# Kernel optimization log

Hardware: AMD Instinct MI355X
Metric: run time of the kernel (lower is better)

Reference implementation:

```python
import jax, jax.numpy as jnp
import numpy as np

B_, L_, H_, P_ = 8, 4096, 512, 256
DT_MIN, DT_MAX = 1e-3, 1e-1


def setup_inputs() -> dict:
    key = jax.random.key(0)
    ks = jax.random.split(key, 6)
    input_sequence = jax.random.normal(ks[0], (B_, L_, H_), jnp.float32)
    # Stable diagonal SSM eigenvalues (HiPPO-like): negative real, spread imaginary
    Lambda_re = -0.5 * jnp.ones((P_,), jnp.float32)
    Lambda_im = jnp.pi * jnp.arange(P_, dtype=jnp.float32)
    # B, C stored as real arrays with trailing real/imag channel, as in the module
    B = jax.random.normal(ks[1], (P_, H_, 2), jnp.float32) / np.sqrt(2.0 * H_)
    C = jax.random.normal(ks[2], (H_, P_, 2), jnp.float32) / np.sqrt(float(P_))
    D = jax.random.normal(ks[3], (H_,), jnp.float32)
    log_step = jax.random.uniform(ks[4], (P_,), jnp.float32,
                                  float(np.log(DT_MIN)), float(np.log(DT_MAX)))
    return dict(input_sequence=input_sequence, Lambda_re=Lambda_re,
                Lambda_im=Lambda_im, B=B, C=C, D=D, log_step=log_step)


def _scan_ssm(Lambda_bar, Bu):
    """Diagonal linear recurrence x_k = Lambda_bar * x_{k-1} + Bu_k via parallel scan.
    Lambda_bar: (P,) complex64; Bu: (L, P) complex64 -> xs: (L, P) complex64."""
    A = jnp.broadcast_to(Lambda_bar, Bu.shape)

    def binop(e_i, e_j):
        a_i, b_i = e_i
        a_j, b_j = e_j
        return a_j * a_i, a_j * b_i + b_j

    _, xs = jax.lax.associative_scan(binop, (A, Bu))
    return xs


def reference(input_sequence, Lambda_re, Lambda_im, B, C, D, log_step):
    # complex parameters (conj_sym=True, clip_eigs=False, zoh discretization)
    Lambda = (Lambda_re + 1j * Lambda_im).astype(jnp.complex64)        # (P,)
    B_tilde = (B[..., 0] + 1j * B[..., 1]).astype(jnp.complex64)       # (P, H)
    C_tilde = (C[..., 0] + 1j * C[..., 1]).astype(jnp.complex64)       # (H, P)
    step = jnp.exp(log_step)                                           # (P,)
    # ZOH: Lambda_bar = exp(Lambda*dt); B_bar = Lambda^{-1}(Lambda_bar - I) B
    Lambda_bar = jnp.exp(Lambda * step)                                # (P,)
    B_bar = ((1.0 / Lambda) * (Lambda_bar - 1.0))[:, None] * B_tilde   # (P, H)
    # project inputs into state space: (B, L, P)
    Bu = jnp.einsum('blh,ph->blp', input_sequence.astype(jnp.complex64), B_bar)
    xs = jax.vmap(lambda bu: _scan_ssm(Lambda_bar, bu))(Bu)            # (B, L, P)
    state = xs[:, -1, :]                                               # (B, P)
    # conj_sym=True -> output uses 2 * Re(C x)
    ys = 2.0 * jnp.einsum('blp,hp->blh', xs, C_tilde).real             # (B, L, H)
    out = ys + D * input_sequence                                      # D-skip
    return out, state
```

## Files before the change

### kernel.cpp

```cpp
#include <hip/hip_runtime.h>
#include <hip/hip_bf16.h>

#define Hh 512
#define Pp 256
#define Ll 4096
#define Bb 8
#define BL (Bb*Ll)
#define Sc 64
#define NC 64

typedef __attribute__((ext_vector_type(8))) __bf16 bf16x8;
typedef __attribute__((ext_vector_type(4))) float  floatx4;

#define LAM_OFF     0
#define LAMS64D_OFF 512
#define B1G_OFF     1024
#define B3G_OFF     (B1G_OFF + 65536)
#define UB16_OFF    (B3G_OFF + 65536)
#define BUB_OFF     (UB16_OFF + 4194304)
#define XSB_OFF     (BUB_OFF + 4194304)
#define AGG_OFF     (XSB_OFF + 4194304)

#define LAMS16D_OFF XSB_OFF
#define AGG16_OFF   (XSB_OFF + 512)

#define OUT_ELEMS 16777216

#define GLL16(g, l) __builtin_amdgcn_global_load_lds( \
    (const __attribute__((address_space(1))) void*)(g), \
    (__attribute__((address_space(3))) void*)(l), 16, 0, 0)

#define BAR_LGKM()  asm volatile("s_waitcnt lgkmcnt(0)\n\ts_barrier" ::: "memory")
#define BAR_VMN(n)  asm volatile("s_waitcnt vmcnt(" #n ")\n\ts_barrier" ::: "memory")

__device__ __forceinline__ float2 cmul(float2 a, float2 b) {
    return make_float2(a.x*b.x - a.y*b.y, a.x*b.y + a.y*b.x);
}
__device__ __forceinline__ void cfma(float2& acc, float2 a, float2 b) {
    acc.x = fmaf(a.x, b.x, acc.x); acc.x = fmaf(-a.y, b.y, acc.x);
    acc.y = fmaf(a.x, b.y, acc.y); acc.y = fmaf( a.y, b.x, acc.y);
}

__global__ void prep(const float* __restrict__ u,
                     const float* __restrict__ Bmat, const float* __restrict__ Cmat,
                     const float* __restrict__ Lre, const float* __restrict__ Lim,
                     const float* __restrict__ logstep, float2* __restrict__ ws) {
    int bid = blockIdx.x;
    if (bid < 8192) {
        long i = ((long)bid * 256 + threadIdx.x) * 8;
        float4 v0 = *(const float4*)(u + i);
        float4 v1 = *(const float4*)(u + i + 4);
        __align__(16) __hip_bfloat162 t[4];
        t[0] = __float22bfloat162_rn(make_float2(v0.x, v0.y));
        t[1] = __float22bfloat162_rn(make_float2(v0.z, v0.w));
        t[2] = __float22bfloat162_rn(make_float2(v1.x, v1.y));
        t[3] = __float22bfloat162_rn(make_float2(v1.z, v1.w));
        *(bf16x8*)((__hip_bfloat16*)(ws + UB16_OFF) + i) = *(const bf16x8*)t;
    } else if (bid < 8704) {
        int idx = (bid - 8192) * 256 + threadIdx.x;
        int p = idx >> 9, h = idx & 511;
        double lr = (double)Lre[p], li = (double)Lim[p];
        double st = exp((double)logstep[p]);
        double a  = lr * st, th = li * st;
        double er = exp(a);
        double lamr = er * cos(th), lami = er * sin(th);
        double nr = lamr - 1.0, ni = lami;
        double den = lr*lr + li*li;
        float gx = (float)((nr*lr + ni*li)/den), gy = (float)((ni*lr - nr*li)/den);
        float2 b = ((const float2*)Bmat)[idx];
        float re = gx*b.x - gy*b.y;
        float im = gx*b.y + gy*b.x;
        __hip_bfloat16* B1 = (__hip_bfloat16*)(ws + B1G_OFF);
        B1[(2*p)*512 + h]   = __float2bfloat16(re);
        B1[(2*p+1)*512 + h] = __float2bfloat16(im);
    } else if (bid < 9216) {
        int idx = (bid - 8704) * 256 + threadIdx.x;
        int h = idx >> 8, p = idx & 255;
        float2 c = ((const float2*)Cmat)[idx];
        __hip_bfloat162* B3 = (__hip_bfloat162*)(ws + B3G_OFF);
        B3[h*256 + p] = __float22bfloat162_rn(make_float2(2.f*c.x, -2.f*c.y));
    } else {
        int p = threadIdx.x;
        double lr = (double)Lre[p], li = (double)Lim[p];
        double st = exp((double)logstep[p]);
        double a  = lr * st, th = li * st;
        double er = exp(a);
        ws[LAM_OFF + p] = make_float2((float)(er*cos(th)), (float)(er*sin(th)));
        double er64 = exp(64.0 * a), th64 = 64.0 * th;
        ((double2*)(ws + LAMS64D_OFF))[p] = make_double2(er64*cos(th64), er64*sin(th64));
        double er16 = exp(16.0 * a), th16 = 16.0 * th;
        ((double2*)(ws + LAMS16D_OFF))[p] = make_double2(er16*cos(th16), er16*sin(th16));
    }
}

#define STAGE(buf, kt) do { \
    _Pragma("unroll") \
    for (int h_ = 0; h_ < 2; ++h_) { \
        _Pragma("unroll") \
        for (int r_ = 0; r_ < 2; ++r_) { \
            GLL16(aSrc + (h_*128 + r_*64)*1024 + (kt)*128, \
                  ldsSt + (buf)*65536 + h_*16384 + r_*8192); \
            GLL16(bSrc + (h_*128 + r_*64)*1024 + (kt)*128, \
                  ldsSt + (buf)*65536 + 32768 + h_*16384 + r_*8192); \
        } \
    } \
} while (0)

__global__ __launch_bounds__(512, 2)
void gemm1(const __hip_bfloat16* __restrict__ A,
           const __hip_bfloat16* __restrict__ B,
           void* __restrict__ Cout,
           const float2* __restrict__ lamTab,
           float2* __restrict__ aggOut,
           float2* __restrict__ agg16Out) {
    __shared__ __align__(16) char lds[131072];
    const int tid = threadIdx.x;
    const int w = tid >> 6, l = tid & 63;

    const int idx = blockIdx.x;
    const int swz = (idx & 7) * 32 + (idx >> 3);
    const int mt = swz >> 1, nt = swz & 1;
    const long M0 = (long)mt * 256;
    const int  N0 = nt * 256;

    const int rA  = l >> 3;
    const int csw = ((l & 7) ^ rA) * 16;
    const char* aSrc = (const char*)A + (M0 + w*8 + rA) * 1024 + csw;
    const char* bSrc = (const char*)B + (long)(N0 + w*8 + rA) * 1024 + csw;
    char* ldsSt = lds + w*1024 + l*16;

    const int quad = l >> 4, ml = l & 15, m7 = ml & 7;
    const int wm = w & 1, wn = w >> 1;
    const int o0 = ((quad    ) ^ m7) * 16;
    const int o1 = ((quad + 4) ^ m7) * 16;
    const char* aRd = lds + wm*16384 + ml*128;
    const char* bRd = lds + 32768 + wn*8192 + ml*128;

    floatx4 acc[8][4];
    #pragma unroll
    for (int i = 0; i < 8; ++i)
        #pragma unroll
        for (int j = 0; j < 4; ++j) acc[i][j] = (floatx4)0.f;

    STAGE(0, 0);
    STAGE(1, 1);
    BAR_VMN(8);

    #pragma unroll
    for (int t = 0; t < 8; ++t) {
        const int tb = (t & 1) * 65536;
        {
            bf16x8 af[8], bfr[4];
            #pragma unroll
            for (int fm = 0; fm < 8; ++fm)
                af[fm] = *(const bf16x8*)(aRd + tb + fm*2048 + o0);
            #pragma unroll
            for (int fn = 0; fn < 4; ++fn)
                bfr[fn] = *(const bf16x8*)(bRd + tb + fn*2048 + o0);
            __builtin_amdgcn_s_setprio(1);
            #pragma unroll
            for (int fm = 0; fm < 8; ++fm)
                #pragma unroll
                for (int fn = 0; fn < 4; ++fn)
                    acc[fm][fn] = __builtin_amdgcn_mfma_f32_16x16x32_bf16(
                        af[fm], bfr[fn], acc[fm][fn], 0, 0, 0);
            __builtin_amdgcn_s_setprio(0);
        }
        {
            bf16x8 af[8], bfr[4];
            #pragma unroll
            for (int fm = 0; fm < 8; ++fm)
                af[fm] = *(const bf16x8*)(aRd + tb + fm*2048 + o1);
            #pragma unroll
            for (int fn = 0; fn < 4; ++fn)
                bfr[fn] = *(const bf16x8*)(bRd + tb + fn*2048 + o1);
            BAR_LGKM();
            if (t + 2 < 8) STAGE(t & 1, t + 2);
            __builtin_amdgcn_sched_barrier(0);
            __builtin_amdgcn_s_setprio(1);
            #pragma unroll
            for (int fm = 0; fm < 8; ++fm)
                #pragma unroll
                for (int fn = 0; fn < 4; ++fn)
                    acc[fm][fn] = __builtin_amdgcn_mfma_f32_16x16x32_bf16(
                        af[fm], bfr[fn], acc[fm][fn], 0, 0, 0);
            __builtin_amdgcn_s_setprio(0);
        }
        if (t < 6)       BAR_VMN(8);
        else if (t == 6) BAR_VMN(0);
    }

    __syncthreads();
    __hip_bfloat16* ldsC = (__hip_bfloat16*)lds;
    const int b   = (int)(M0 >> 12);
    const int gc0 = (int)((M0 >> 6) & 63);
    #pragma unroll
    for (int fn = 0; fn < 4; ++fn) {
        const int col = N0 + wn*64 + fn*16 + ml;
        const int cl  = wn*64 + fn*16 + ml;
        const int p = col >> 1;
        const float2 lam = lamTab[p];
        const float2 one = make_float2(1.f, 0.f);
        const float2 l2  = cmul(lam, lam);
        const float2 l3  = cmul(l2, lam);
        const float2 l4  = cmul(l2, l2);
        const float2 l8  = cmul(l4, l4);
        const float2 l12 = cmul(l8, l4);
        const float2 l16 = cmul(l8, l8);
        const float2 l32 = cmul(l16, l16);
        const float2 l48 = cmul(l32, l16);
        const float2 P4q = (quad==3) ? one : (quad==2) ? l4 : (quad==1) ? l8 : l12;
        #pragma unroll
        for (int c = 0; c < 2; ++c) {
            float2 sc = make_float2(0.f, 0.f);
            #pragma unroll
            for (int a = 0; a < 4; ++a) {
                const int fm = c*4 + a;
                float vr[4];
                #pragma unroll
                for (int reg = 0; reg < 4; ++reg) {
                    const int rl = wm*128 + fm*16 + quad*4 + reg;
                    __hip_bfloat16 hv = __float2bfloat16(acc[fm][fn][reg]);
                    ldsC[rl*256 + cl] = hv;
                    vr[reg] = __bfloat162float(hv);
                }
                float2 s;
                s.x = fmaf(l3.x, vr[0], fmaf(l2.x, vr[1], fmaf(lam.x, vr[2], vr[3])));
                s.y = fmaf(l3.y, vr[0], fmaf(l2.y, vr[1], lam.y * vr[2]));
                const float2 p16 = (a==3) ? one : (a==2) ? l16 : (a==1) ? l32 : l48;
                cfma(sc, cmul(p16, P4q), s);
                float2 tq = cmul(P4q, s);
                tq.x += __shfl_xor(tq.x, 16); tq.y += __shfl_xor(tq.y, 16);
                tq.x += __shfl_xor(tq.x, 32); tq.y += __shfl_xor(tq.y, 32);
                const float tox = __shfl_xor(tq.x, 1);
                const float toy = __shfl_xor(tq.y, 1);
                if (quad == 0 && (ml & 1) == 0)
                    agg16Out[((size_t)((b*NC + gc0 + wm*2 + c)*4 + a))*Pp + p] =
                        make_float2(tq.x - toy, tq.y + tox);
            }
            sc.x += __shfl_xor(sc.x, 16); sc.y += __shfl_xor(sc.y, 16);
            sc.x += __shfl_xor(sc.x, 32); sc.y += __shfl_xor(sc.y, 32);
            const float ox = __shfl_xor(sc.x, 1);
            const float oy = __shfl_xor(sc.y, 1);
            if (quad == 0 && (ml & 1) == 0) {
                aggOut[(b*NC + gc0 + wm*2 + c) * Pp + p] =
                    make_float2(sc.x - oy, sc.y + ox);
            }
        }
    }
    __syncthreads();
    {
        const int rr = tid >> 5;
        const int cb = (tid & 31) * 16;
        #pragma unroll
        for (int pass = 0; pass < 16; ++pass) {
            const int r = pass * 16 + rr;
            *(float4*)((char*)Cout + (M0 + r) * 1024 + (long)N0 * 2 + cb) =
                *(const float4*)(lds + r * 512 + cb);
        }
    }
}

#define STAGEA2(buf, kt) do { \
    _Pragma("unroll") \
    for (int h_ = 0; h_ < 2; ++h_) { \
        _Pragma("unroll") \
        for (int r_ = 0; r_ < 2; ++r_) { \
            GLL16(aSrc + (h_*128 + r_*64)*1024 + (kt)*128, \
                  ldsA + (buf)*32768 + h_*16384 + r_*8192); \
        } \
    } \
} while (0)
#define STAGEB2(buf, kt) do { \
    _Pragma("unroll") \
    for (int h_ = 0; h_ < 2; ++h_) { \
        _Pragma("unroll") \
        for (int r_ = 0; r_ < 2; ++r_) { \
            GLL16(bSrc + (h_*128 + r_*64)*1024 + (kt)*128, \
                  ldsB + (buf)*32768 + h_*16384 + r_*8192); \
        } \
    } \
} while (0)

#define SCAN_TILE(ktC, bufA) do { \
    const int s16_ = tid >> 5; \
    const float2 lam_ = lamK[ktC]; \
    float2 x_ = carry16L[s16_*256 + (ktC)*32 + p5g]; \
    char* base_ = lds + (bufA)*32768; \
    float2 v_[16]; \
    _Pragma("unroll") \
    for (int jj_ = 0; jj_ < 16; ++jj_) { \
        const int j_ = (s16_ << 4) + jj_; \
        v_[jj_] = __bfloat1622float2(*(const __hip_bfloat162*)(base_ + j_*128 + \
            ((((p5g >> 2) ^ (j_ & 7)) << 4) | ((p5g & 3) << 2)))); \
    } \
    _Pragma("unroll") \
    for (int jj_ = 0; jj_ < 16; ++jj_) { \
        const int j_ = (s16_ << 4) + jj_; \
        float nr_ = fmaf(lam_.x, x_.x, v_[jj_].x); nr_ = fmaf(-lam_.y, x_.y, nr_); \
        float ni_ = fmaf(lam_.x, x_.y, v_[jj_].y); ni_ = fmaf( lam_.y, x_.x, ni_); \
        x_.x = nr_; x_.y = ni_; \
        *(__hip_bfloat162*)(base_ + j_*128 + \
            ((((p5g >> 2) ^ (j_ & 7)) << 4) | ((p5g & 3) << 2))) = \
            __float22bfloat162_rn(x_); \
    } \
    if (s16_ == 15 && gc0 == 60 && nt == 0) { \
        out[OUT_ELEMS + b * Pp + (ktC)*32 + p5g] = x_.x; \
        out[OUT_ELEMS + Bb * Pp + b * Pp + (ktC)*32 + p5g] = x_.y; \
    } \
} while (0)

__global__ __launch_bounds__(512, 2)
void gemm2f(const __hip_bfloat16* __restrict__ A,
            const __hip_bfloat16* __restrict__ Bg,
            float* __restrict__ out,
            const __hip_bfloat16* __restrict__ ub,
            const float* __restrict__ Dv,
            const float2* __restrict__ lamTab,
            const double2* __restrict__ lam64,
            const double2* __restrict__ lam16,
            const float2* __restrict__ agg,
            const float2* __restrict__ agg16) {
    __shared__ __align__(16) char lds[163840];
    const int tid = threadIdx.x;
    const int w = tid >> 6, l = tid & 63;
    const int idx = blockIdx.x;
    const int swz = (idx & 7) * 32 + (idx >> 3);
    const int mt = swz >> 1, nt = swz & 1;
    const long M0 = (long)mt * 256;
    const int  N0 = nt * 256;
    const int b   = (int)(M0 >> 12);
    const int gc0 = (int)((M0 >> 6) & 63);

    const int rA  = l >> 3;
    const int csw = ((l & 7) ^ rA) * 16;
    const char* aSrc = (const char*)A + (M0 + w*8 + rA) * 1024 + csw;
    const char* bSrc = (const char*)Bg + (long)(N0 + w*8 + rA) * 1024 + csw;
    char* ldsA = lds + w*1024 + l*16;
    char* ldsB = lds + 65536 + w*1024 + l*16;

    const int quad = l >> 4, ml = l & 15, m7 = ml & 7;
    const int wm = w & 1, wn = w >> 1;
    const int o0 = ((quad    ) ^ m7) * 16;
    const int o1 = ((quad + 4) ^ m7) * 16;
    const char* aRd = lds + wm*16384 + ml*128;
    const char* bRd = lds + 65536 + wn*8192 + ml*128;
    float2* carry16L = (float2*)(lds + 131072);

    const int p5g = tid & 31;
    float2 lamK[8];
    #pragma unroll
    for (int kt = 0; kt < 8; ++kt) lamK[kt] = lamTab[kt*32 + p5g];

    STAGEA2(0, 0); STAGEB2(0, 0);
    STAGEA2(1, 1); STAGEB2(1, 1);

    if (tid < 256) {
        const int p = tid;
        const double2 l64 = lam64[p];
        const double2 l16 = lam16[p];
        double cr = 0.0, ci = 0.0;
        for (int cp = 0; cp + 4 <= gc0; cp += 4) {
            float2 a0 = agg[(b*NC + cp    ) * Pp + p];
            float2 a1 = agg[(b*NC + cp + 1) * Pp + p];
            float2 a2 = agg[(b*NC + cp + 2) * Pp + p];
            float2 a3 = agg[(b*NC + cp + 3) * Pp + p];
            double nr, ni;
            nr = fma(l64.x, cr, (double)a0.x); nr = fma(-l64.y, ci, nr);
            ni = fma(l64.x, ci, (double)a0.y); ni = fma( l64.y, cr, ni); cr = nr; ci = ni;
            nr = fma(l64.x, cr, (double)a1.x); nr = fma(-l64.y, ci, nr);
            ni = fma(l64.x, ci, (double)a1.y); ni = fma( l64.y, cr, ni); cr = nr; ci = ni;
            nr = fma(l64.x, cr, (double)a2.x); nr = fma(-l64.y, ci, nr);
            ni = fma(l64.x, ci, (double)a2.y); ni = fma( l64.y, cr, ni); cr = nr; ci = ni;
            nr = fma(l64.x, cr, (double)a3.x); nr = fma(-l64.y, ci, nr);
            ni = fma(l64.x, ci, (double)a3.y); ni = fma( l64.y, cr, ni); cr = nr; ci = ni;
        }
        #pragma unroll
        for (int ch = 0; ch < 4; ++ch) {
            carry16L[(ch*4 + 0)*256 + p] = make_float2((float)cr, (float)ci);
            double scr = cr, sci = ci;
            #pragma unroll
            for (int sq = 1; sq < 4; ++sq) {
                float2 a16 = agg16[((size_t)((b*NC + gc0 + ch)*4 + (sq-1)))*Pp + p];
                double nr = fma(l16.x, scr, (double)a16.x); nr = fma(-l16.y, sci, nr);
                double ni = fma(l16.x, sci, (double)a16.y); ni = fma( l16.y, scr, ni);
                scr = nr; sci = ni;
                carry16L[(ch*4 + sq)*256 + p] = make_float2((float)scr, (float)sci);
            }
            if (ch < 3) {
                float2 a = agg[(b*NC + gc0 + ch) * Pp + p];
                double nr = fma(l64.x, cr, (double)a.x); nr = fma(-l64.y, ci, nr);
                double ni = fma(l64.x, ci, (double)a.y); ni = fma( l64.y, cr, ni);
                cr = nr; ci = ni;
            }
        }
    }
    asm volatile("s_waitcnt vmcnt(8) lgkmcnt(0)\n\ts_barrier" ::: "memory");
    SCAN_TILE(0, 0);
    BAR_LGKM();

    floatx4 acc[8][4];
    #pragma unroll
    for (int i = 0; i < 8; ++i)
        #pragma unroll
        for (int j = 0; j < 4; ++j) acc[i][j] = (floatx4)0.f;

    #pragma unroll
    for (int kt = 0; kt < 8; ++kt) {
        const int cb = kt & 1;
        const int tb = cb * 32768;
        {
            bf16x8 af[8], bfr[4];
            #pragma unroll
            for (int fm = 0; fm < 8; ++fm)
                af[fm] = *(const bf16x8*)(aRd + tb + fm*2048 + o0);
            #pragma unroll
            for (int fn = 0; fn < 4; ++fn)
                bfr[fn] = *(const bf16x8*)(bRd + tb + fn*2048 + o0);
            __builtin_amdgcn_s_setprio(1);
            #pragma unroll
            for (int fm = 0; fm < 8; ++fm)
                #pragma unroll
                for (int fn = 0; fn < 4; ++fn)
                    acc[fm][fn] = __builtin_amdgcn_mfma_f32_16x16x32_bf16(
                        af[fm], bfr[fn], acc[fm][fn], 0, 0, 0);
            __builtin_amdgcn_s_setprio(0);
        }
        {
            bf16x8 af[8], bfr[4];
            #pragma unroll
            for (int fm = 0; fm < 8; ++fm)
                af[fm] = *(const bf16x8*)(aRd + tb + fm*2048 + o1);
            #pragma unroll
            for (int fn = 0; fn < 4; ++fn)
                bfr[fn] = *(const bf16x8*)(bRd + tb + fn*2048 + o1);
            BAR_LGKM();
            if (kt + 2 < 8) { STAGEA2(cb, kt + 2); STAGEB2(cb, kt + 2); }
            __builtin_amdgcn_sched_barrier(0);
            __builtin_amdgcn_s_setprio(1);
            #pragma unroll
            for (int fm = 0; fm < 8; ++fm)
                #pragma unroll
                for (int fn = 0; fn < 4; ++fn)
                    acc[fm][fn] = __builtin_amdgcn_mfma_f32_16x16x32_bf16(
                        af[fm], bfr[fn], acc[fm][fn], 0, 0, 0);
            __builtin_amdgcn_s_setprio(0);
        }
        if (kt < 6)       { BAR_VMN(8); SCAN_TILE(kt + 1, cb ^ 1); BAR_LGKM(); }
        else if (kt == 6) { BAR_VMN(0); SCAN_TILE(7, cb ^ 1); BAR_LGKM(); }
    }

    #pragma unroll
    for (int fm = 0; fm < 8; ++fm)
        #pragma unroll
        for (int fn = 0; fn < 4; ++fn) {
            const int col = N0 + wn*64 + fn*16 + ml;
            const float d = Dv[col];
            #pragma unroll
            for (int reg = 0; reg < 4; ++reg) {
                const long row = M0 + wm*128 + fm*16 + quad*4 + reg;
                const long o = row * 512 + col;
                out[o] = acc[fm][fn][reg] + d * __bfloat162float(ub[o]);
            }
        }
}

extern "C" void kernel_launch(void* const* d_in, const int* in_sizes, int n_in,
                              void* d_out, int out_size, void* d_ws, size_t ws_size,
                              hipStream_t stream) {
    const float* u       = (const float*)d_in[0];
    const float* Lre     = (const float*)d_in[1];
    const float* Lim     = (const float*)d_in[2];
    const float* Bmat    = (const float*)d_in[3];
    const float* Cmat    = (const float*)d_in[4];
    const float* Dv      = (const float*)d_in[5];
    const float* logstep = (const float*)d_in[6];
    float*  out = (float*)d_out;
    float2* ws  = (float2*)d_ws;

    prep<<<9217, 256, 0, stream>>>(u, Bmat, Cmat, Lre, Lim, logstep, ws);

    gemm1<<<256, 512, 0, stream>>>(
        (const __hip_bfloat16*)(ws + UB16_OFF),
        (const __hip_bfloat16*)(ws + B1G_OFF),
        (void*)(ws + BUB_OFF),
        (const float2*)(ws + LAM_OFF),
        (float2*)(ws + AGG_OFF),
        (float2*)(ws + AGG16_OFF));

    gemm2f<<<256, 512, 0, stream>>>(
        (const __hip_bfloat16*)(ws + BUB_OFF),
        (const __hip_bfloat16*)(ws + B3G_OFF),
        out,
        (const __hip_bfloat16*)(ws + UB16_OFF), Dv,
        (const float2*)(ws + LAM_OFF),
        (const double2*)(ws + LAMS64D_OFF),
        (const double2*)(ws + LAMS16D_OFF),
        (const float2*)(ws + AGG_OFF),
        (const float2*)(ws + AGG16_OFF));
}
```

Baseline: 185.4 us.

## Overlap scan tile with MFMA and stage epilogue through LDS for coalesced stores

The scan of the next tile is moved inside the second MFMA sub-step, so it is issued before the matrix multiplies rather than after them. This should let scan work overlap with MFMA execution. The output epilogue now writes accumulators to LDS one half-block at a time, then reads them back row-wise so the D-skip fused store uses float4 writes and 8-byte bf16 loads instead of scattered scalar accesses. This adds extra barriers and LDS traffic, and it reuses the LDS buffer, which could be a hazard if other data is still live there.

```diff
diff --git a/kernel.cpp b/kernel.cpp
--- a/kernel.cpp
+++ b/kernel.cpp
@@ -437,6 +437,8 @@
             BAR_LGKM();
             if (kt + 2 < 8) { STAGEA2(cb, kt + 2); STAGEB2(cb, kt + 2); }
             __builtin_amdgcn_sched_barrier(0);
+            if (kt < 6)       { BAR_VMN(8); SCAN_TILE(kt + 1, cb ^ 1); }
+            else if (kt == 6) { BAR_VMN(0); SCAN_TILE(7, cb ^ 1); }
             __builtin_amdgcn_s_setprio(1);
             #pragma unroll
             for (int fm = 0; fm < 8; ++fm)
@@ -445,24 +447,46 @@
                     acc[fm][fn] = __builtin_amdgcn_mfma_f32_16x16x32_bf16(
                         af[fm], bfr[fn], acc[fm][fn], 0, 0, 0);
             __builtin_amdgcn_s_setprio(0);
-        }
-        if (kt < 6)       { BAR_VMN(8); SCAN_TILE(kt + 1, cb ^ 1); BAR_LGKM(); }
-        else if (kt == 6) { BAR_VMN(0); SCAN_TILE(7, cb ^ 1); BAR_LGKM(); }
-    }
-
-    #pragma unroll
-    for (int fm = 0; fm < 8; ++fm)
+            if (kt < 7) BAR_LGKM();
+        }
+    }
+
+    __syncthreads();
+    float* ldsC = (float*)lds;
+    const int er = tid >> 6;
+    const int ec = (tid & 63) * 4;
+    #pragma unroll
+    for (int half = 0; half < 2; ++half) {
+        if (wm == half) {
+            #pragma unroll
+            for (int fm = 0; fm < 8; ++fm)
+                #pragma unroll
+                for (int fn = 0; fn < 4; ++fn) {
+                    const int cl = wn*64 + fn*16 + ml;
+                    #pragma unroll
+                    for (int reg = 0; reg < 4; ++reg)
+                        ldsC[(fm*16 + quad*4 + reg)*256 + cl] = acc[fm][fn][reg];
+                }
+        }
+        __syncthreads();
         #pragma unroll
-        for (int fn = 0; fn < 4; ++fn) {
-            const int col = N0 + wn*64 + fn*16 + ml;
-            const float d = Dv[col];
-            #pragma unroll
-            for (int reg = 0; reg < 4; ++reg) {
-                const long row = M0 + wm*128 + fm*16 + quad*4 + reg;
-                const long o = row * 512 + col;
-                out[o] = acc[fm][fn][reg] + d * __bfloat162float(ub[o]);
-            }
-        }
+        for (int g = 0; g < 16; ++g) {
+            const int rl = g*8 + er;
+            const long row = M0 + half*128 + rl;
+            float4 v = *(const float4*)(ldsC + rl*256 + ec);
+            const __hip_bfloat16* up = ub + row*512 + N0 + ec;
+            float2 f01 = __bfloat1622float2(*(const __hip_bfloat162*)up);
+            float2 f23 = __bfloat1622float2(*(const __hip_bfloat162*)(up + 2));
+            float4 dv = *(const float4*)(Dv + N0 + ec);
+            float4 o;
+            o.x = fmaf(dv.x, f01.x, v.x);
+            o.y = fmaf(dv.y, f01.y, v.y);
+            o.z = fmaf(dv.z, f23.x, v.z);
+            o.w = fmaf(dv.w, f23.y, v.w);
+            *(float4*)(out + row*512 + N0 + ec) = o;
+        }
+        __syncthreads();
+    }
 }
 
 extern "C" void kernel_launch(void* const* d_in, const int* in_sizes, int n_in,
```

After: 191.0 us. +3.0%, slower.

## Shrink gemm2f tiles to 128x128 and launch four times as many blocks

Applied to the files above, without the earlier changes.

The fused scan+GEMM kernel now uses 128x128 output tiles instead of 256x256, with 1024 blocks, half the LDS and launch bounds raised to 4 blocks per CU. The carry setup, staging, scan (now done by half the threads) and final-state write are all adjusted to the smaller 128-row chunk. This aims to fill the GPU better (256 blocks previously underfilled the CUs) and improve latency hiding. In exchange there is less operand reuse per block, more redundant carry-prefix computation across blocks, and only half the threads do the serial scan.

```diff
diff --git a/kernel.cpp b/kernel.cpp
--- a/kernel.cpp
+++ b/kernel.cpp
@@ -261,56 +261,50 @@
     }
 }
 
-#define STAGEA2(buf, kt) do { \
+#define STAGEA3(buf, kt) do { \
     _Pragma("unroll") \
     for (int h_ = 0; h_ < 2; ++h_) { \
+        GLL16(aSrc + (h_*64)*1024 + (kt)*128, ldsA + (buf)*16384 + h_*8192); \
+    } \
+} while (0)
+#define STAGEB3(buf, kt) do { \
+    _Pragma("unroll") \
+    for (int h_ = 0; h_ < 2; ++h_) { \
+        GLL16(bSrc + (h_*64)*1024 + (kt)*128, ldsB + (buf)*16384 + h_*8192); \
+    } \
+} while (0)
+
+#define SCAN3(ktC, bufA) do { \
+    if (tid < 256) { \
+        const int s16_ = tid >> 5;            \
+        const float2 lam_ = lamK[ktC]; \
+        float2 x_ = carry16L[s16_*256 + (ktC)*32 + p5g]; \
+        char* base_ = lds + (bufA)*16384; \
+        float2 v_[16]; \
         _Pragma("unroll") \
-        for (int r_ = 0; r_ < 2; ++r_) { \
-            GLL16(aSrc + (h_*128 + r_*64)*1024 + (kt)*128, \
-                  ldsA + (buf)*32768 + h_*16384 + r_*8192); \
+        for (int jj_ = 0; jj_ < 16; ++jj_) { \
+            const int j_ = (s16_ << 4) + jj_; \
+            v_[jj_] = __bfloat1622float2(*(const __hip_bfloat162*)(base_ + j_*128 + \
+                ((((p5g >> 2) ^ (j_ & 7)) << 4) | ((p5g & 3) << 2)))); \
+        } \
+        _Pragma("unroll") \
+        for (int jj_ = 0; jj_ < 16; ++jj_) { \
+            const int j_ = (s16_ << 4) + jj_; \
+            float nr_ = fmaf(lam_.x, x_.x, v_[jj_].x); nr_ = fmaf(-lam_.y, x_.y, nr_); \
+            float ni_ = fmaf(lam_.x, x_.y, v_[jj_].y); ni_ = fmaf( lam_.y, x_.x, ni_); \
+            x_.x = nr_; x_.y = ni_; \
+            *(__hip_bfloat162*)(base_ + j_*128 + \
+                ((((p5g >> 2) ^ (j_ & 7)) << 4) | ((p5g & 3) << 2))) = \
+                __float22bfloat162_rn(x_); \
+        } \
+        if (s16_ == 7 && gc0 == 62 && nt == 0) { \
+            out[OUT_ELEMS + b * Pp + (ktC)*32 + p5g] = x_.x; \
+            out[OUT_ELEMS + Bb * Pp + b * Pp + (ktC)*32 + p5g] = x_.y; \
         } \
     } \
 } while (0)
-#define STAGEB2(buf, kt) do { \
-    _Pragma("unroll") \
-    for (int h_ = 0; h_ < 2; ++h_) { \
-        _Pragma("unroll") \
-        for (int r_ = 0; r_ < 2; ++r_) { \
-            GLL16(bSrc + (h_*128 + r_*64)*1024 + (kt)*128, \
-                  ldsB + (buf)*32768 + h_*16384 + r_*8192); \
-        } \
-    } \
-} while (0)
-
-#define SCAN_TILE(ktC, bufA) do { \
-    const int s16_ = tid >> 5; \
-    const float2 lam_ = lamK[ktC]; \
-    float2 x_ = carry16L[s16_*256 + (ktC)*32 + p5g]; \
-    char* base_ = lds + (bufA)*32768; \
-    float2 v_[16]; \
-    _Pragma("unroll") \
-    for (int jj_ = 0; jj_ < 16; ++jj_) { \
-        const int j_ = (s16_ << 4) + jj_; \
-        v_[jj_] = __bfloat1622float2(*(const __hip_bfloat162*)(base_ + j_*128 + \
-            ((((p5g >> 2) ^ (j_ & 7)) << 4) | ((p5g & 3) << 2)))); \
-    } \
-    _Pragma("unroll") \
-    for (int jj_ = 0; jj_ < 16; ++jj_) { \
-        const int j_ = (s16_ << 4) + jj_; \
-        float nr_ = fmaf(lam_.x, x_.x, v_[jj_].x); nr_ = fmaf(-lam_.y, x_.y, nr_); \
-        float ni_ = fmaf(lam_.x, x_.y, v_[jj_].y); ni_ = fmaf( lam_.y, x_.x, ni_); \
-        x_.x = nr_; x_.y = ni_; \
-        *(__hip_bfloat162*)(base_ + j_*128 + \
-            ((((p5g >> 2) ^ (j_ & 7)) << 4) | ((p5g & 3) << 2))) = \
-            __float22bfloat162_rn(x_); \
-    } \
-    if (s16_ == 15 && gc0 == 60 && nt == 0) { \
-        out[OUT_ELEMS + b * Pp + (ktC)*32 + p5g] = x_.x; \
-        out[OUT_ELEMS + Bb * Pp + b * Pp + (ktC)*32 + p5g] = x_.y; \
-    } \
-} while (0)
-
-__global__ __launch_bounds__(512, 2)
+
+__global__ __launch_bounds__(512, 4)
 void gemm2f(const __hip_bfloat16* __restrict__ A,
             const __hip_bfloat16* __restrict__ Bg,
             float* __restrict__ out,
@@ -321,14 +315,14 @@
             const double2* __restrict__ lam16,
             const float2* __restrict__ agg,
             const float2* __restrict__ agg16) {
-    __shared__ __align__(16) char lds[163840];
+    __shared__ __align__(16) char lds[81920];
     const int tid = threadIdx.x;
     const int w = tid >> 6, l = tid & 63;
     const int idx = blockIdx.x;
-    const int swz = (idx & 7) * 32 + (idx >> 3);
-    const int mt = swz >> 1, nt = swz & 1;
-    const long M0 = (long)mt * 256;
-    const int  N0 = nt * 256;
+    const int swz = (idx & 7) * 128 + (idx >> 3);
+    const int mt = swz >> 2, nt = swz & 3;
+    const long M0 = (long)mt * 128;
+    const int  N0 = nt * 128;
     const int b   = (int)(M0 >> 12);
     const int gc0 = (int)((M0 >> 6) & 63);
 
@@ -337,46 +331,40 @@
     const char* aSrc = (const char*)A + (M0 + w*8 + rA) * 1024 + csw;
     const char* bSrc = (const char*)Bg + (long)(N0 + w*8 + rA) * 1024 + csw;
     char* ldsA = lds + w*1024 + l*16;
-    char* ldsB = lds + 65536 + w*1024 + l*16;
+    char* ldsB = lds + 32768 + w*1024 + l*16;
 
     const int quad = l >> 4, ml = l & 15, m7 = ml & 7;
     const int wm = w & 1, wn = w >> 1;
     const int o0 = ((quad    ) ^ m7) * 16;
     const int o1 = ((quad + 4) ^ m7) * 16;
-    const char* aRd = lds + wm*16384 + ml*128;
-    const char* bRd = lds + 65536 + wn*8192 + ml*128;
-    float2* carry16L = (float2*)(lds + 131072);
+    const char* aRd = lds + wm*8192 + ml*128;
+    const char* bRd = lds + 32768 + wn*4096 + ml*128;
+    float2* carry16L = (float2*)(lds + 65536);
 
     const int p5g = tid & 31;
     float2 lamK[8];
     #pragma unroll
     for (int kt = 0; kt < 8; ++kt) lamK[kt] = lamTab[kt*32 + p5g];
 
-    STAGEA2(0, 0); STAGEB2(0, 0);
-    STAGEA2(1, 1); STAGEB2(1, 1);
+    STAGEA3(0, 0); STAGEB3(0, 0);
+    STAGEA3(1, 1); STAGEB3(1, 1);
 
     if (tid < 256) {
         const int p = tid;
         const double2 l64 = lam64[p];
         const double2 l16 = lam16[p];
         double cr = 0.0, ci = 0.0;
-        for (int cp = 0; cp + 4 <= gc0; cp += 4) {
+        for (int cp = 0; cp + 2 <= gc0; cp += 2) {
             float2 a0 = agg[(b*NC + cp    ) * Pp + p];
             float2 a1 = agg[(b*NC + cp + 1) * Pp + p];
-            float2 a2 = agg[(b*NC + cp + 2) * Pp + p];
-            float2 a3 = agg[(b*NC + cp + 3) * Pp + p];
             double nr, ni;
             nr = fma(l64.x, cr, (double)a0.x); nr = fma(-l64.y, ci, nr);
             ni = fma(l64.x, ci, (double)a0.y); ni = fma( l64.y, cr, ni); cr = nr; ci = ni;
             nr = fma(l64.x, cr, (double)a1.x); nr = fma(-l64.y, ci, nr);
             ni = fma(l64.x, ci, (double)a1.y); ni = fma( l64.y, cr, ni); cr = nr; ci = ni;
-            nr = fma(l64.x, cr, (double)a2.x); nr = fma(-l64.y, ci, nr);
-            ni = fma(l64.x, ci, (double)a2.y); ni = fma( l64.y, cr, ni); cr = nr; ci = ni;
-            nr = fma(l64.x, cr, (double)a3.x); nr = fma(-l64.y, ci, nr);
-            ni = fma(l64.x, ci, (double)a3.y); ni = fma( l64.y, cr, ni); cr = nr; ci = ni;
-        }
-        #pragma unroll
-        for (int ch = 0; ch < 4; ++ch) {
+        }
+        #pragma unroll
+        for (int ch = 0; ch < 2; ++ch) {
             carry16L[(ch*4 + 0)*256 + p] = make_float2((float)cr, (float)ci);
             double scr = cr, sci = ci;
             #pragma unroll
@@ -387,7 +375,7 @@
                 scr = nr; sci = ni;
                 carry16L[(ch*4 + sq)*256 + p] = make_float2((float)scr, (float)sci);
             }
-            if (ch < 3) {
+            if (ch < 1) {
                 float2 a = agg[(b*NC + gc0 + ch) * Pp + p];
                 double nr = fma(l64.x, cr, (double)a.x); nr = fma(-l64.y, ci, nr);
                 double ni = fma(l64.x, ci, (double)a.y); ni = fma( l64.y, cr, ni);
@@ -395,70 +383,70 @@
             }
         }
     }
-    asm volatile("s_waitcnt vmcnt(8) lgkmcnt(0)\n\ts_barrier" ::: "memory");
-    SCAN_TILE(0, 0);
+    asm volatile("s_waitcnt vmcnt(4) lgkmcnt(0)\n\ts_barrier" ::: "memory");
+    SCAN3(0, 0);
     BAR_LGKM();
 
-    floatx4 acc[8][4];
-    #pragma unroll
-    for (int i = 0; i < 8; ++i)
-        #pragma unroll
-        for (int j = 0; j < 4; ++j) acc[i][j] = (floatx4)0.f;
+    floatx4 acc[4][2];
+    #pragma unroll
+    for (int i = 0; i < 4; ++i)
+        #pragma unroll
+        for (int j = 0; j < 2; ++j) acc[i][j] = (floatx4)0.f;
 
     #pragma unroll
     for (int kt = 0; kt < 8; ++kt) {
         const int cb = kt & 1;
-        const int tb = cb * 32768;
+        const int tb = cb * 16384;
         {
-            bf16x8 af[8], bfr[4];
-            #pragma unroll
-            for (int fm = 0; fm < 8; ++fm)
+            bf16x8 af[4], bfr[2];
+            #pragma unroll
+            for (int fm = 0; fm < 4; ++fm)
                 af[fm] = *(const bf16x8*)(aRd + tb + fm*2048 + o0);
             #pragma unroll
-            for (int fn = 0; fn < 4; ++fn)
+            for (int fn = 0; fn < 2; ++fn)
                 bfr[fn] = *(const bf16x8*)(bRd + tb + fn*2048 + o0);
             __builtin_amdgcn_s_setprio(1);
             #pragma unroll
-            for (int fm = 0; fm < 8; ++fm)
+            for (int fm = 0; fm < 4; ++fm)
                 #pragma unroll
-                for (int fn = 0; fn < 4; ++fn)
+                for (int fn = 0; fn < 2; ++fn)
                     acc[fm][fn] = __builtin_amdgcn_mfma_f32_16x16x32_bf16(
                         af[fm], bfr[fn], acc[fm][fn], 0, 0, 0);
             __builtin_amdgcn_s_setprio(0);
         }
         {
-            bf16x8 af[8], bfr[4];
-            #pragma unroll
-            for (int fm = 0; fm < 8; ++fm)
+            bf16x8 af[4], bfr[2];
+            #pragma unroll
+            for (int fm = 0; fm < 4; ++fm)
                 af[fm] = *(const bf16x8*)(aRd + tb + fm*2048 + o1);
             #pragma unroll
-            for (int fn = 0; fn < 4; ++fn)
+            for (int fn = 0; fn < 2; ++fn)
                 bfr[fn] = *(const bf16x8*)(bRd + tb + fn*2048 + o1);
             BAR_LGKM();
-            if (kt + 2 < 8) { STAGEA2(cb, kt + 2); STAGEB2(cb, kt + 2); }
+            if (kt + 2 < 8) { STAGEA3(cb, kt + 2); STAGEB3(cb, kt + 2); }
             __builtin_amdgcn_sched_barrier(0);
             __builtin_amdgcn_s_setprio(1);
             #pragma unroll
-            for (int fm = 0; fm < 8; ++fm)
+            for (int fm = 0; fm < 4; ++fm)
                 #pragma unroll
-                for (int fn = 0; fn < 4; ++fn)
+                for (int fn = 0; fn < 2; ++fn)
                     acc[fm][fn] = __builtin_amdgcn_mfma_f32_16x16x32_bf16(
                         af[fm], bfr[fn], acc[fm][fn], 0, 0, 0);
             __builtin_amdgcn_s_setprio(0);
         }
-        if (kt < 6)       { BAR_VMN(8); SCAN_TILE(kt + 1, cb ^ 1); BAR_LGKM(); }
-        else if (kt == 6) { BAR_VMN(0); SCAN_TILE(7, cb ^ 1); BAR_LGKM(); }
-    }
-
-    #pragma unroll
-    for (int fm = 0; fm < 8; ++fm)
-        #pragma unroll
-        for (int fn = 0; fn < 4; ++fn) {
-            const int col = N0 + wn*64 + fn*16 + ml;
+        if (kt < 6)       { BAR_VMN(4); SCAN3(kt + 1, cb ^ 1); BAR_LGKM(); }
+        else if (kt == 6) { BAR_VMN(0); SCAN3(7, cb ^ 1); BAR_LGKM(); }
+    }
+
+    #pragma unroll
+    for (int fm = 0; fm < 4; ++fm)
+        #pragma unroll
+        for (int fn = 0; fn < 2; ++fn) {
+            const int col = N0 + wn*32 + fn*16 + ml;
             const float d = Dv[col];
             #pragma unroll
             for (int reg = 0; reg < 4; ++reg) {
-                const long row = M0 + wm*128 + fm*16 + quad*4 + reg;
+                const long row = M0 + wm*64 + fm*16 + quad*4 + reg;
                 const long o = row * 512 + col;
                 out[o] = acc[fm][fn][reg] + d * __bfloat162float(ub[o]);
             }
@@ -488,7 +476,7 @@
         (float2*)(ws + AGG_OFF),
         (float2*)(ws + AGG16_OFF));
 
-    gemm2f<<<256, 512, 0, stream>>>(
+    gemm2f<<<1024, 512, 0, stream>>>(
         (const __hip_bfloat16*)(ws + BUB_OFF),
         (const __hip_bfloat16*)(ws + B3G_OFF),
         out,
```

Measured after the change: 191.5 us. +3.3%, slower.
